# Kernel tuning notes

Hardware: AMD Instinct MI355X
Metric: run time of the kernel (lower is better)

Reference implementation:

```python
import jax, jax.numpy as jnp
import numpy as np

B, L, H, N2, NLAYERS = 8, 4096, 256, 32, 4


def setup_inputs() -> dict:
    key = jax.random.key(0)
    ks = jax.random.split(key, 7)
    x = jax.random.normal(ks[0], (B, L, H), dtype=jnp.float32)
    # S4D kernel params (per layer, stacked on leading dim)
    dt_min, dt_max = 1e-3, 1e-1
    u = jax.random.uniform(ks[1], (NLAYERS, H), dtype=jnp.float32)
    log_dt = u * (np.log(dt_max) - np.log(dt_min)) + np.log(dt_min)
    log_A_real = jnp.log(0.5 * jnp.ones((NLAYERS, H, N2), jnp.float32))
    A_imag = jnp.broadcast_to(np.pi * jnp.arange(N2, dtype=jnp.float32), (NLAYERS, H, N2)) * jnp.ones((NLAYERS, H, N2), jnp.float32)
    C_re = jax.random.normal(ks[2], (NLAYERS, H, N2), dtype=jnp.float32) * (0.5 ** 0.5)
    C_im = jax.random.normal(ks[3], (NLAYERS, H, N2), dtype=jnp.float32) * (0.5 ** 0.5)
    D = jax.random.normal(ks[4], (NLAYERS, H), dtype=jnp.float32)
    Wout = jax.random.normal(ks[5], (NLAYERS, 2 * H, H), dtype=jnp.float32) * (1.0 / H) ** 0.5
    bout = jnp.zeros((NLAYERS, 2 * H), jnp.float32)
    ln_g = jnp.ones((NLAYERS, H), jnp.float32)
    ln_b = jnp.zeros((NLAYERS, H), jnp.float32)
    return dict(x=x, log_dt=log_dt, log_A_real=log_A_real, A_imag=A_imag,
                C_re=C_re, C_im=C_im, D=D, Wout=Wout, bout=bout,
                ln_g=ln_g, ln_b=ln_b)


def _s4d_kernel(log_dt, log_A_real, A_imag, C_re, C_im, Lseq):
    # Vandermonde kernel of S4D: k[h,l] = 2*Re sum_n C'_hn exp(dt_h*A_hn*l)
    dt = jnp.exp(log_dt)                       # (H,)
    A = (-jnp.exp(log_A_real) + 1j * A_imag)   # (H,N) complex
    C = C_re + 1j * C_im                       # (H,N)
    dtA = A * dt[:, None]                      # (H,N)
    K = jnp.exp(dtA[:, :, None] * jnp.arange(Lseq, dtype=jnp.float32))  # (H,N,L)
    Cm = C * (jnp.exp(dtA) - 1.0) / A          # ZOH discretization of C
    return 2.0 * jnp.einsum('hn,hnl->hl', Cm, K).real  # (H,L)


def _s4d_layer(u, log_dt, log_A_real, A_imag, C_re, C_im, D, Wout, bout):
    # u: (B,H,L)
    Lq = u.shape[-1]
    k = _s4d_kernel(log_dt, log_A_real, A_imag, C_re, C_im, Lq)  # (H,L)
    kf = jnp.fft.rfft(k, n=2 * Lq)             # (H, L+1)
    uf = jnp.fft.rfft(u, n=2 * Lq)             # (B,H,L+1)
    y = jnp.fft.irfft(uf * kf, n=2 * Lq)[..., :Lq]
    y = y + u * D[:, None]
    y = jax.nn.gelu(y, approximate=False)
    # output linear: 1x1 conv H->2H followed by GLU along channel dim
    y = jnp.einsum('oh,bhl->bol', Wout, y) + bout[None, :, None]
    a, b = jnp.split(y, 2, axis=1)
    return a * jax.nn.sigmoid(b)               # (B,H,L)


def _layernorm_ch(x, g, b, eps=1e-5):
    # x: (B,H,L); normalize over channel axis H (matches norm on (B,L,H))
    m = jnp.mean(x, axis=1, keepdims=True)
    v = jnp.mean((x - m) ** 2, axis=1, keepdims=True)
    return (x - m) / jnp.sqrt(v + eps) * g[None, :, None] + b[None, :, None]


def reference(x, log_dt, log_A_real, A_imag, C_re, C_im, D, Wout, bout, ln_g, ln_b):
    u = jnp.swapaxes(x, -1, -2)  # (B,H,L)
    for i in range(NLAYERS):  # post-norm (prenorm=False), dropout=identity (eval)
        z = _s4d_layer(u, log_dt[i], log_A_real[i], A_imag[i], C_re[i], C_im[i],
                       D[i], Wout[i], bout[i])
        u = z + u
        u = _layernorm_ch(u, ln_g[i], ln_b[i])
    return jnp.swapaxes(u, -1, -2)  # (B,L,H)
```

## Files before the change

### kernel.cpp

```cpp
#include <hip/hip_runtime.h>
#include <math.h>

#define B    8
#define L    4096
#define H    256
#define N2   32
#define NL   4
#define O2   512
#define BLK  64
#define NBLK 64
#define TVP  136
#define MJP  72
#define UTP  72
#define INP  68
#define TL2  64
#define YPAD 264
#define URP  72

typedef __attribute__((ext_vector_type(8))) short short8;
typedef __attribute__((ext_vector_type(4))) float f32x4;

__device__ __forceinline__ unsigned short f2bf(float f)
{
    unsigned int u = __float_as_uint(f);
    unsigned int r = (u + 0x7fffu + ((u >> 16) & 1u)) >> 16;
    return (unsigned short)r;
}

__device__ __forceinline__ float bf2f(unsigned short v)
{
    return __uint_as_float(((unsigned int)v) << 16);
}

__device__ __forceinline__ float gelu_f(float x)
{
    float t = 1.59576912161f * fmaf(0.044715f * x * x, x, x);
    return x / (1.f + __expf(-t));
}

__global__ __launch_bounds__(256) void k_setup(
    const float* __restrict__ x, const float* __restrict__ log_dt,
    const float* __restrict__ log_Ar, const float* __restrict__ A_im,
    const float* __restrict__ C_re, const float* __restrict__ C_im,
    const float* __restrict__ Dv, const float* __restrict__ Wout,
    unsigned short* __restrict__ Wb, unsigned short* __restrict__ TVc,
    unsigned short* __restrict__ Mm, float2* __restrict__ w64c,
    unsigned short* __restrict__ u)
{
    __shared__ __align__(16) unsigned char smem_raw[27648];
    const int bid = blockIdx.x;
    const int t = threadIdx.x;

    if (bid < 512) {
        int idx = (bid * 256 + t) * 4;
        float4 v = *(const float4*)(Wout + idx);
        ushort4 o;
        o.x = f2bf(v.x); o.y = f2bf(v.y); o.z = f2bf(v.z); o.w = f2bf(v.w);
        *(ushort4*)(Wb + idx) = o;
    } else if (bid < 1536) {
        unsigned short* tvS = (unsigned short*)smem_raw;
        unsigned short* mmS = tvS + BLK * TVP;
        float* kbS = (float*)(mmS + BLK * MJP);
        float* cS  = kbS + BLK;
        const int id = bid - 512;
        const int layer = id >> 8, h = id & 255;
        if (t < 32) {
            const int n0 = t;
            const int idx = (layer * H + h) * N2 + n0;
            double dt = exp((double)log_dt[layer * H + h]);
            double Ar = -exp((double)log_Ar[idx]);
            double Ai = (double)A_im[idx];
            double dtr = dt * Ar, dti = dt * Ai;
            double er = exp(dtr);
            double dwr = er * cos(dti), dwi = er * sin(dti);
            double numr = dwr - 1.0, numi = dwi;
            double den = Ar * Ar + Ai * Ai;
            double qr0 = (numr * Ar + numi * Ai) / den;
            double qi0 = (numi * Ar - numr * Ai) / den;
            double dcr = (double)C_re[idx], dci = (double)C_im[idx];
            cS[n0]       = (float)(2.0 * (dcr * qr0 - dci * qi0));
            cS[32 + n0]  = (float)(2.0 * (dcr * qi0 + dci * qr0));
            cS[64 + n0]  = (float)dwr;
            cS[96 + n0]  = (float)dwi;
            double rev = dti * 0.15915494309189535;
            cS[128 + n0] = (float)(rev - floor(rev));
            cS[160 + n0] = (float)dtr;
            double m64 = exp(64.0 * dtr);
            double a64 = 64.0 * dti;
            w64c[(layer * H + h) * N2 + n0] =
                make_float2((float)(m64 * cos(a64)), (float)(m64 * sin(a64)));
        }
        __syncthreads();
        const int n = t & 31, dg = t >> 5;
        const float cr = cS[n], ci = cS[32 + n];
        const float wr = cS[64 + n], wi = cS[96 + n];
        const float revf = cS[128 + n], dtrf = cS[160 + n];
#pragma unroll
        for (int i = 0; i < 8; ++i) {
            const int d = dg * 8 + i;
            float ph = (float)d * revf;
            ph = (ph - floorf(ph)) * 6.28318530718f;
            float mag = __expf((float)d * dtrf);
            float vr = mag * __cosf(ph);
            float vi = mag * __sinf(ph);
            float pk = fmaf(cr, vr, -(ci * vi));
            pk += __shfl_xor(pk, 1);  pk += __shfl_xor(pk, 2);
            pk += __shfl_xor(pk, 4);  pk += __shfl_xor(pk, 8);
            pk += __shfl_xor(pk, 16);
            if (n == 0) kbS[d] = pk;
            mmS[n * MJP + (63 - d)]        = f2bf(vr);
            mmS[(32 + n) * MJP + (63 - d)] = f2bf(vi);
            float v1r = vr * wr - vi * wi;
            float v1i = vr * wi + vi * wr;
            tvS[d * TVP + 64 + n] = f2bf(fmaf(cr, v1r, -(ci * v1i)));
            tvS[d * TVP + 96 + n] = f2bf(-fmaf(cr, v1i, ci * v1r));
        }
        __syncthreads();
        {
            const int r = t >> 2, c0 = (t & 3) * 16;
            const float diag = kbS[0] + Dv[layer * H + h];
            short8 o8[2];
#pragma unroll
            for (int j = 0; j < 16; ++j) {
                int c = c0 + j;
                float val = (c > r) ? 0.f : ((c == r) ? diag : kbS[r - c]);
                o8[j >> 3][j & 7] = (short)f2bf(val);
            }
            *(short8*)&tvS[r * TVP + c0]     = o8[0];
            *(short8*)&tvS[r * TVP + c0 + 8] = o8[1];
        }
        __syncthreads();
        unsigned short* tv = TVc + (size_t)(layer * H + h) * BLK * TVP;
        unsigned short* mm = Mm + (size_t)(layer * H + h) * BLK * MJP;
        for (int c = t; c < (BLK * TVP) / 8; c += 256)
            *(short8*)(tv + c * 8) = *(const short8*)&tvS[c * 8];
        for (int c = t; c < (BLK * MJP) / 8; c += 256)
            *(short8*)(mm + c * 8) = *(const short8*)&mmS[c * 8];
    } else {
        float* sh = (float*)smem_raw;
        const int rb = bid - 1536;
        const int hx = rb & 7, ly = (rb >> 3) & 63, b = rb >> 9;
        const int h0 = hx * 32, l0 = ly * 64;
        const int tx = t & 7, ty = t >> 3;
        const float* xb = x + ((size_t)b * L + l0) * H + h0;
#pragma unroll
        for (int i = 0; i < 2; ++i) {
            int l = ty + i * 32;
            float4 v = *(const float4*)(xb + (size_t)l * H + tx * 4);
            sh[(tx * 4 + 0) * 68 + l] = v.x;
            sh[(tx * 4 + 1) * 68 + l] = v.y;
            sh[(tx * 4 + 2) * 68 + l] = v.z;
            sh[(tx * 4 + 3) * 68 + l] = v.w;
        }
        __syncthreads();
        const int hh = t >> 3, cc = (t & 7) * 8;
        const float* row = &sh[hh * 68 + cc];
        short8 o8;
#pragma unroll
        for (int j = 0; j < 8; ++j) o8[j] = (short)f2bf(row[j]);
        *(short8*)(u + ((size_t)b * H + h0 + hh) * L + l0 + cc) = o8;
    }
}

__global__ __launch_bounds__(256) void k_scan3(
    const unsigned short* __restrict__ u, const unsigned short* __restrict__ Mm_l,
    const unsigned short* __restrict__ TVc_l, const float2* __restrict__ w64c_l,
    unsigned short* __restrict__ y)
{
    __shared__ __align__(16) unsigned short uT[BLK * UTP];
    __shared__ __align__(16) unsigned short ST[BLK * UTP];
    __shared__ __align__(16) float INC[BLK * INP];
    __shared__ float2 cLd[4][32];
    const int t = threadIdx.x;
    const int wv = t >> 6, lane = t & 63;
    const int lanei = lane & 15, quad = lane >> 4;
    const int h = blockIdx.x >> 3, ct = blockIdx.x & 7;
    const unsigned short* ub = u + (size_t)(ct * H + h) * L;

    const unsigned short* arowA = Mm_l + (size_t)h * BLK * MJP + (wv * 16 + lanei) * MJP + quad * 8;
    short8 mA[2];
    mA[0] = *(const short8*)(arowA);
    mA[1] = *(const short8*)(arowA + 32);
    const unsigned short* arowB = TVc_l + (size_t)h * BLK * TVP + (wv * 16 + lanei) * TVP + quad * 8;
    short8 tB[4];
#pragma unroll
    for (int kt = 0; kt < 4; ++kt)
        tB[kt] = *(const short8*)(arowB + kt * 32);
    const float2 w64 = w64c_l[h * N2 + (lane & 31)];

    {
        int col = t >> 2, q = t & 3;
        *(short8*)&uT[col * UTP + q * 16]     = *(const short8*)(ub + col * 64 + q * 16);
        *(short8*)&uT[col * UTP + q * 16 + 8] = *(const short8*)(ub + col * 64 + q * 16 + 8);
    }
    __syncthreads();

    {
        f32x4 acc[4];
#pragma unroll
        for (int nt = 0; nt < 4; ++nt) acc[nt] = (f32x4){0.f, 0.f, 0.f, 0.f};
#pragma unroll
        for (int kt = 0; kt < 2; ++kt) {
#pragma unroll
            for (int nt = 0; nt < 4; ++nt) {
                short8 b8 = *(const short8*)&uT[(nt * 16 + lanei) * UTP + kt * 32 + quad * 8];
                acc[nt] = __builtin_amdgcn_mfma_f32_16x16x32_bf16(mA[kt], b8, acc[nt], 0, 0, 0);
            }
        }
#pragma unroll
        for (int nt = 0; nt < 4; ++nt)
            *(f32x4*)&INC[(nt * 16 + lanei) * INP + wv * 16 + quad * 4] = acc[nt];
    }
    __syncthreads();

    const int n = lane & 31;
    float Pr[16], Pi[16];
    float w1r = 1.f, w1i = 0.f;
    if (lane < 32) {
        float sr = 0.f, si = 0.f;
        const int base = wv * 16;
#pragma unroll
        for (int k = 0; k < 16; ++k) {
            Pr[k] = sr; Pi[k] = si;
            float ir = INC[(base + k) * INP + n];
            float ii = INC[(base + k) * INP + 32 + n];
            float nr = fmaf(w64.x, sr, fmaf(-w64.y, si, ir));
            float ni = fmaf(w64.x, si, fmaf(w64.y, sr, ii));
            sr = nr; si = ni;
        }
        cLd[wv][n] = make_float2(sr, si);
        float ar = w64.x, ai = w64.y;
#pragma unroll
        for (int q = 0; q < 4; ++q) {
            float nr2 = ar * ar - ai * ai;
            float ni2 = 2.f * ar * ai;
            ar = nr2; ai = ni2;
        }
        w1r = ar; w1i = ai;
    }
    __syncthreads();
    if (lane < 32) {
        float Cr = 0.f, Ci = 0.f;
        for (int wp = 0; wp < wv; ++wp) {
            float2 Lw = cLd[wp][n];
            float nr = fmaf(w1r, Cr, fmaf(-w1i, Ci, Lw.x));
            float ni = fmaf(w1r, Ci, fmaf(w1i, Cr, Lw.y));
            Cr = nr; Ci = ni;
        }
        float pr = 1.f, pi = 0.f;
#pragma unroll
        for (int k = 0; k < 16; ++k) {
            int blk = wv * 16 + k;
            float Sr = fmaf(pr, Cr, fmaf(-pi, Ci, Pr[k]));
            float Si = fmaf(pr, Ci, fmaf(pi, Cr, Pi[k]));
            ST[blk * UTP + n]      = f2bf(Sr);
            ST[blk * UTP + 32 + n] = f2bf(Si);
            float npr = pr * w64.x - pi * w64.y;
            float npi = pr * w64.y + pi * w64.x;
            pr = npr; pi = npi;
        }
    }
    __syncthreads();

    {
        f32x4 acc[4];
#pragma unroll
        for (int nt = 0; nt < 4; ++nt) acc[nt] = (f32x4){0.f, 0.f, 0.f, 0.f};
#pragma unroll
        for (int kt = 0; kt < 4; ++kt) {
            const unsigned short* bb = (kt < 2) ? uT : ST;
            int ko = (kt & 1) * 32 + quad * 8;
#pragma unroll
            for (int nt = 0; nt < 4; ++nt) {
                short8 b8 = *(const short8*)&bb[(nt * 16 + lanei) * UTP + ko];
                acc[nt] = __builtin_amdgcn_mfma_f32_16x16x32_bf16(tB[kt], b8, acc[nt], 0, 0, 0);
            }
        }
        unsigned short* yb = y + (size_t)(ct * H + h) * L;
#pragma unroll
        for (int nt = 0; nt < 4; ++nt) {
            int blk = nt * 16 + lanei;
            int i0 = wv * 16 + quad * 4;
            ushort4 o4;
            o4.x = f2bf(gelu_f(acc[nt][0]));
            o4.y = f2bf(gelu_f(acc[nt][1]));
            o4.z = f2bf(gelu_f(acc[nt][2]));
            o4.w = f2bf(gelu_f(acc[nt][3]));
            *(ushort4*)(yb + blk * 64 + i0) = o4;
        }
    }
}

__global__ __launch_bounds__(512, 4) void k_gemm(
    const unsigned short* __restrict__ y, unsigned short* __restrict__ u,
    const unsigned short* __restrict__ Wb, const float* __restrict__ bo,
    const float* __restrict__ lng, const float* __restrict__ lnb,
    float* __restrict__ outp)
{
    __shared__ __align__(16) unsigned short yS[H * URP];
    __shared__ float bS[O2];
    __shared__ float lgS[H], lbS[H];
    __shared__ float redS[8][4][16], redQ[8][4][16];

    const int t = threadIdx.x;
    const int wv = t >> 6;
    const int lane = t & 63;
    const int lanei = lane & 15;
    const int quad = lane >> 4;
    const int b = blockIdx.x >> 6;
    const int l0 = (blockIdx.x & 63) * TL2;

    size_t abase[2][2];
#pragma unroll
    for (int p = 0; p < 2; ++p)
#pragma unroll
        for (int jj = 0; jj < 2; ++jj)
            abase[p][jj] = (size_t)(p * 256 + wv * 32 + jj * 16 + lanei) * H + quad * 8;

    short8 a8p[4];
#pragma unroll
    for (int p = 0; p < 2; ++p)
#pragma unroll
        for (int jj = 0; jj < 2; ++jj)
            a8p[p * 2 + jj] = *(const short8*)(Wb + abase[p][jj]);

    {
        const int i = t & 7, hr = t >> 3;
        const unsigned short* yb = y + (size_t)b * H * L + l0 + i * 8;
#pragma unroll
        for (int ps = 0; ps < 4; ++ps) {
            int h = ps * 64 + hr;
            short8 v8 = *(const short8*)(yb + (size_t)h * L);
#pragma unroll
            for (int r = 0; r < 8; ++r)
                yS[(i * 8 + r) * YPAD + (h ^ (8 * i))] = (unsigned short)v8[r];
        }
        if (t < O2) bS[t] = bo[t];
        if (t < H) { lgS[t] = lng[t]; lbS[t] = lnb[t]; }
    }
    __syncthreads();

    f32x4 acc[2][2][4];
#pragma unroll
    for (int p = 0; p < 2; ++p)
#pragma unroll
        for (int jj = 0; jj < 2; ++jj)
#pragma unroll
            for (int nt = 0; nt < 4; ++nt)
                acc[p][jj][nt] = (f32x4){0.f, 0.f, 0.f, 0.f};

#pragma unroll
    for (int kt = 0; kt < 8; ++kt) {
        short8 bfr[4];
#pragma unroll
        for (int nt = 0; nt < 4; ++nt) {
            int lp = nt * 16 + lanei;
            int a = (2 * nt + (lanei >> 3)) & 7;
            bfr[nt] = *(const short8*)&yS[lp * YPAD + ((kt * 32 + quad * 8) ^ (8 * a))];
        }
#pragma unroll
        for (int p = 0; p < 2; ++p)
#pragma unroll
            for (int jj = 0; jj < 2; ++jj) {
                short8 a8 = (kt == 0) ? a8p[p * 2 + jj]
                                      : *(const short8*)(Wb + abase[p][jj] + kt * 32);
#pragma unroll
                for (int nt = 0; nt < 4; ++nt)
                    acc[p][jj][nt] = __builtin_amdgcn_mfma_f32_16x16x32_bf16(
                        a8, bfr[nt], acc[p][jj][nt], 0, 0, 0);
            }
    }
    __syncthreads();

    unsigned short* ub = u + (size_t)b * H * L + l0;
#pragma unroll
    for (int r = 0; r < 4; ++r) {
        int c = r * 512 + t;
        int o = c >> 3, c8 = (c & 7) * 8;
        *(short8*)&yS[o * URP + c8] = *(const short8*)(ub + (size_t)o * L + c8);
    }
    __syncthreads();

    float psum[4] = {0.f, 0.f, 0.f, 0.f}, psq[4] = {0.f, 0.f, 0.f, 0.f};
#pragma unroll
    for (int jj = 0; jj < 2; ++jj) {
#pragma unroll
        for (int nt = 0; nt < 4; ++nt) {
            int lc = nt * 16 + lanei;
#pragma unroll
            for (int reg = 0; reg < 4; ++reg) {
                int o = wv * 32 + jj * 16 + quad * 4 + reg;
                float a = acc[0][jj][nt][reg] + bS[o];
                float g = acc[1][jj][nt][reg] + bS[o + 256];
                float glu = a / (1.f + __expf(-g));
                float val = glu + bf2f(yS[o * URP + lc]);
                acc[0][jj][nt][reg] = val;
                psum[nt] += val;
                psq[nt] = fmaf(val, val, psq[nt]);
            }
        }
    }
#pragma unroll
    for (int nt = 0; nt < 4; ++nt) {
        psum[nt] += __shfl_xor(psum[nt], 16);
        psum[nt] += __shfl_xor(psum[nt], 32);
        psq[nt]  += __shfl_xor(psq[nt], 16);
        psq[nt]  += __shfl_xor(psq[nt], 32);
    }
    if (lane < 16) {
#pragma unroll
        for (int nt = 0; nt < 4; ++nt) {
            redS[wv][nt][lanei] = psum[nt];
            redQ[wv][nt][lanei] = psq[nt];
        }
    }
    __syncthreads();
    float mcol[4], icol[4];
#pragma unroll
    for (int nt = 0; nt < 4; ++nt) {
        float s = 0.f, q = 0.f;
#pragma unroll
        for (int w = 0; w < 8; ++w) { s += redS[w][nt][lanei]; q += redQ[w][nt][lanei]; }
        float m = s * (1.0f / 256.0f);
        float v = q * (1.0f / 256.0f) - m * m;
        mcol[nt] = m;
        icol[nt] = rsqrtf(v + 1e-5f);
    }
    if (outp == nullptr) {
#pragma unroll
        for (int jj = 0; jj < 2; ++jj) {
#pragma unroll
            for (int nt = 0; nt < 4; ++nt) {
                int lc = nt * 16 + lanei;
#pragma unroll
                for (int reg = 0; reg < 4; ++reg) {
                    int o = wv * 32 + jj * 16 + quad * 4 + reg;
                    float val = acc[0][jj][nt][reg];
                    float ov = (val - mcol[nt]) * icol[nt] * lgS[o] + lbS[o];
                    yS[o * URP + lc] = f2bf(ov);
                }
            }
        }
        __syncthreads();
#pragma unroll
        for (int r = 0; r < 4; ++r) {
            int c = r * 512 + t;
            int o = c >> 3, c8 = (c & 7) * 8;
            *(short8*)(ub + (size_t)o * L + c8) = *(const short8*)&yS[o * URP + c8];
        }
    } else {
#pragma unroll
        for (int jj = 0; jj < 2; ++jj) {
#pragma unroll
            for (int nt = 0; nt < 4; ++nt) {
                int lc = nt * 16 + lanei;
                int o0 = wv * 32 + jj * 16 + quad * 4;
                float4 ov;
#pragma unroll
                for (int reg = 0; reg < 4; ++reg) {
                    int o = o0 + reg;
                    float val = acc[0][jj][nt][reg];
                    ((float*)&ov)[reg] = (val - mcol[nt]) * icol[nt] * lgS[o] + lbS[o];
                }
                *(float4*)(outp + ((size_t)b * L + l0 + lc) * H + o0) = ov;
            }
        }
    }
}

extern "C" void kernel_launch(void* const* d_in, const int* in_sizes, int n_in,
                              void* d_out, int out_size, void* d_ws, size_t ws_size,
                              hipStream_t stream)
{
    const float* x      = (const float*)d_in[0];
    const float* log_dt = (const float*)d_in[1];
    const float* log_Ar = (const float*)d_in[2];
    const float* A_im   = (const float*)d_in[3];
    const float* C_re   = (const float*)d_in[4];
    const float* C_im   = (const float*)d_in[5];
    const float* Dv     = (const float*)d_in[6];
    const float* Wout   = (const float*)d_in[7];
    const float* bout   = (const float*)d_in[8];
    const float* lng    = (const float*)d_in[9];
    const float* lnb    = (const float*)d_in[10];
    float* out = (float*)d_out;

    unsigned short* u   = (unsigned short*)d_ws;
    unsigned short* Wb  = u + (size_t)B * H * L;
    unsigned short* TVc = Wb + (size_t)NL * O2 * H;
    unsigned short* Mm  = TVc + (size_t)NL * H * BLK * TVP;
    float2* w64c        = (float2*)(Mm + (size_t)NL * H * BLK * MJP);
    unsigned short* y   = (unsigned short*)(w64c + (size_t)NL * H * N2);

    k_setup<<<5632, 256, 0, stream>>>(x, log_dt, log_Ar, A_im, C_re, C_im, Dv, Wout,
                                      Wb, TVc, Mm, w64c, u);
    for (int layer = 0; layer < NL; ++layer) {
        k_scan3<<<H * 8, 256, 0, stream>>>(u, Mm + (size_t)layer * H * BLK * MJP,
                                           TVc + (size_t)layer * H * BLK * TVP,
                                           w64c + (size_t)layer * H * N2, y);
        k_gemm<<<B * L / TL2, 512, 0, stream>>>(y, u, Wb + (size_t)layer * O2 * H,
                                                bout + layer * O2, lng + layer * H, lnb + layer * H,
                                                (layer == NL - 1) ? out : nullptr);
    }
}
```

Baseline: 298.9 us.

## Halve GEMM L-tile to 32 with 256-thread blocks; stage scan output via LDS

The GEMM/GLU/LayerNorm kernel now uses 32-column L tiles with 256 threads, each wave covering 64 output channels. That doubles the grid and cuts per-block LDS, which may raise occupancy, but W is reloaded twice as often. The scan kernel now writes its gelu output to shared memory and stores it to global as coalesced 16-byte vectors instead of scattered 8-byte stores. This adds two barriers.

```diff
diff --git a/kernel.cpp b/kernel.cpp
--- a/kernel.cpp
+++ b/kernel.cpp
@@ -13,9 +13,9 @@
 #define MJP  72
 #define UTP  72
 #define INP  68
-#define TL2  64
+#define TL2  32
 #define YPAD 264
-#define URP  72
+#define URP2 40
 
 typedef __attribute__((ext_vector_type(8))) short short8;
 typedef __attribute__((ext_vector_type(4))) float f32x4;
@@ -276,7 +276,7 @@
                 acc[nt] = __builtin_amdgcn_mfma_f32_16x16x32_bf16(tB[kt], b8, acc[nt], 0, 0, 0);
             }
         }
-        unsigned short* yb = y + (size_t)(ct * H + h) * L;
+        __syncthreads();
 #pragma unroll
         for (int nt = 0; nt < 4; ++nt) {
             int blk = nt * 16 + lanei;
@@ -286,46 +286,47 @@
             o4.y = f2bf(gelu_f(acc[nt][1]));
             o4.z = f2bf(gelu_f(acc[nt][2]));
             o4.w = f2bf(gelu_f(acc[nt][3]));
-            *(ushort4*)(yb + blk * 64 + i0) = o4;
-        }
-    }
-}
-
-__global__ __launch_bounds__(512, 4) void k_gemm(
+            *(ushort4*)&uT[blk * UTP + i0] = o4;
+        }
+        __syncthreads();
+        unsigned short* yb = y + (size_t)(ct * H + h) * L;
+#pragma unroll
+        for (int r = 0; r < 2; ++r) {
+            int c = r * 256 + t;
+            int o = c >> 3, c8 = (c & 7) * 8;
+            *(short8*)(yb + o * 64 + c8) = *(const short8*)&uT[o * UTP + c8];
+        }
+    }
+}
+
+__global__ __launch_bounds__(256, 4) void k_gemm(
     const unsigned short* __restrict__ y, unsigned short* __restrict__ u,
     const unsigned short* __restrict__ Wb, const float* __restrict__ bo,
     const float* __restrict__ lng, const float* __restrict__ lnb,
     float* __restrict__ outp)
 {
-    __shared__ __align__(16) unsigned short yS[H * URP];
+    __shared__ __align__(16) unsigned short yS[10240];
     __shared__ float bS[O2];
     __shared__ float lgS[H], lbS[H];
-    __shared__ float redS[8][4][16], redQ[8][4][16];
+    __shared__ float redS[4][2][16], redQ[4][2][16];
 
     const int t = threadIdx.x;
     const int wv = t >> 6;
     const int lane = t & 63;
     const int lanei = lane & 15;
     const int quad = lane >> 4;
-    const int b = blockIdx.x >> 6;
-    const int l0 = (blockIdx.x & 63) * TL2;
-
-    size_t abase[2][2];
+    const int b = blockIdx.x >> 7;
+    const int l0 = (blockIdx.x & 127) * TL2;
+
+    size_t abase[2][4];
 #pragma unroll
     for (int p = 0; p < 2; ++p)
 #pragma unroll
-        for (int jj = 0; jj < 2; ++jj)
-            abase[p][jj] = (size_t)(p * 256 + wv * 32 + jj * 16 + lanei) * H + quad * 8;
-
-    short8 a8p[4];
-#pragma unroll
-    for (int p = 0; p < 2; ++p)
-#pragma unroll
-        for (int jj = 0; jj < 2; ++jj)
-            a8p[p * 2 + jj] = *(const short8*)(Wb + abase[p][jj]);
+        for (int jj = 0; jj < 4; ++jj)
+            abase[p][jj] = (size_t)(p * 256 + wv * 64 + jj * 16 + lanei) * H + quad * 8;
 
     {
-        const int i = t & 7, hr = t >> 3;
+        const int i = t & 3, hr = t >> 2;
         const unsigned short* yb = y + (size_t)b * H * L + l0 + i * 8;
 #pragma unroll
         for (int ps = 0; ps < 4; ++ps) {
@@ -335,25 +336,26 @@
             for (int r = 0; r < 8; ++r)
                 yS[(i * 8 + r) * YPAD + (h ^ (8 * i))] = (unsigned short)v8[r];
         }
-        if (t < O2) bS[t] = bo[t];
-        if (t < H) { lgS[t] = lng[t]; lbS[t] = lnb[t]; }
-    }
-    __syncthreads();
-
-    f32x4 acc[2][2][4];
+        bS[t] = bo[t];
+        bS[t + 256] = bo[t + 256];
+        lgS[t] = lng[t]; lbS[t] = lnb[t];
+    }
+    __syncthreads();
+
+    f32x4 acc[2][4][2];
 #pragma unroll
     for (int p = 0; p < 2; ++p)
 #pragma unroll
-        for (int jj = 0; jj < 2; ++jj)
-#pragma unroll
-            for (int nt = 0; nt < 4; ++nt)
+        for (int jj = 0; jj < 4; ++jj)
+#pragma unroll
+            for (int nt = 0; nt < 2; ++nt)
                 acc[p][jj][nt] = (f32x4){0.f, 0.f, 0.f, 0.f};
 
 #pragma unroll
     for (int kt = 0; kt < 8; ++kt) {
-        short8 bfr[4];
-#pragma unroll
-        for (int nt = 0; nt < 4; ++nt) {
+        short8 bfr[2];
+#pragma unroll
+        for (int nt = 0; nt < 2; ++nt) {
             int lp = nt * 16 + lanei;
             int a = (2 * nt + (lanei >> 3)) & 7;
             bfr[nt] = *(const short8*)&yS[lp * YPAD + ((kt * 32 + quad * 8) ^ (8 * a))];
@@ -361,11 +363,10 @@
 #pragma unroll
         for (int p = 0; p < 2; ++p)
 #pragma unroll
-            for (int jj = 0; jj < 2; ++jj) {
-                short8 a8 = (kt == 0) ? a8p[p * 2 + jj]
-                                      : *(const short8*)(Wb + abase[p][jj] + kt * 32);
-#pragma unroll
-                for (int nt = 0; nt < 4; ++nt)
+            for (int jj = 0; jj < 4; ++jj) {
+                short8 a8 = *(const short8*)(Wb + abase[p][jj] + kt * 32);
+#pragma unroll
+                for (int nt = 0; nt < 2; ++nt)
                     acc[p][jj][nt] = __builtin_amdgcn_mfma_f32_16x16x32_bf16(
                         a8, bfr[nt], acc[p][jj][nt], 0, 0, 0);
             }
@@ -375,25 +376,25 @@
     unsigned short* ub = u + (size_t)b * H * L + l0;
 #pragma unroll
     for (int r = 0; r < 4; ++r) {
-        int c = r * 512 + t;
-        int o = c >> 3, c8 = (c & 7) * 8;
-        *(short8*)&yS[o * URP + c8] = *(const short8*)(ub + (size_t)o * L + c8);
-    }
-    __syncthreads();
-
-    float psum[4] = {0.f, 0.f, 0.f, 0.f}, psq[4] = {0.f, 0.f, 0.f, 0.f};
-#pragma unroll
-    for (int jj = 0; jj < 2; ++jj) {
-#pragma unroll
-        for (int nt = 0; nt < 4; ++nt) {
+        int c = r * 256 + t;
+        int o = c >> 2, c8 = (c & 3) * 8;
+        *(short8*)&yS[o * URP2 + c8] = *(const short8*)(ub + (size_t)o * L + c8);
+    }
+    __syncthreads();
+
+    float psum[2] = {0.f, 0.f}, psq[2] = {0.f, 0.f};
+#pragma unroll
+    for (int jj = 0; jj < 4; ++jj) {
+#pragma unroll
+        for (int nt = 0; nt < 2; ++nt) {
             int lc = nt * 16 + lanei;
 #pragma unroll
             for (int reg = 0; reg < 4; ++reg) {
-                int o = wv * 32 + jj * 16 + quad * 4 + reg;
+                int o = wv * 64 + jj * 16 + quad * 4 + reg;
                 float a = acc[0][jj][nt][reg] + bS[o];
                 float g = acc[1][jj][nt][reg] + bS[o + 256];
                 float glu = a / (1.f + __expf(-g));
-                float val = glu + bf2f(yS[o * URP + lc]);
+                float val = glu + bf2f(yS[o * URP2 + lc]);
                 acc[0][jj][nt][reg] = val;
                 psum[nt] += val;
                 psq[nt] = fmaf(val, val, psq[nt]);
@@ -401,7 +402,7 @@
         }
     }
 #pragma unroll
-    for (int nt = 0; nt < 4; ++nt) {
+    for (int nt = 0; nt < 2; ++nt) {
         psum[nt] += __shfl_xor(psum[nt], 16);
         psum[nt] += __shfl_xor(psum[nt], 32);
         psq[nt]  += __shfl_xor(psq[nt], 16);
@@ -409,18 +410,18 @@
     }
     if (lane < 16) {
 #pragma unroll
-        for (int nt = 0; nt < 4; ++nt) {
+        for (int nt = 0; nt < 2; ++nt) {
             redS[wv][nt][lanei] = psum[nt];
             redQ[wv][nt][lanei] = psq[nt];
         }
     }
     __syncthreads();
-    float mcol[4], icol[4];
-#pragma unroll
-    for (int nt = 0; nt < 4; ++nt) {
+    float mcol[2], icol[2];
+#pragma unroll
+    for (int nt = 0; nt < 2; ++nt) {
         float s = 0.f, q = 0.f;
 #pragma unroll
-        for (int w = 0; w < 8; ++w) { s += redS[w][nt][lanei]; q += redQ[w][nt][lanei]; }
+        for (int w = 0; w < 4; ++w) { s += redS[w][nt][lanei]; q += redQ[w][nt][lanei]; }
         float m = s * (1.0f / 256.0f);
         float v = q * (1.0f / 256.0f) - m * m;
         mcol[nt] = m;
@@ -428,33 +429,33 @@
     }
     if (outp == nullptr) {
 #pragma unroll
-        for (int jj = 0; jj < 2; ++jj) {
-#pragma unroll
-            for (int nt = 0; nt < 4; ++nt) {
+        for (int jj = 0; jj < 4; ++jj) {
+#pragma unroll
+            for (int nt = 0; nt < 2; ++nt) {
                 int lc = nt * 16 + lanei;
 #pragma unroll
                 for (int reg = 0; reg < 4; ++reg) {
-                    int o = wv * 32 + jj * 16 + quad * 4 + reg;
+                    int o = wv * 64 + jj * 16 + quad * 4 + reg;
                     float val = acc[0][jj][nt][reg];
                     float ov = (val - mcol[nt]) * icol[nt] * lgS[o] + lbS[o];
-                    yS[o * URP + lc] = f2bf(ov);
+                    yS[o * URP2 + lc] = f2bf(ov);
                 }
             }
         }
         __syncthreads();
 #pragma unroll
         for (int r = 0; r < 4; ++r) {
-            int c = r * 512 + t;
-            int o = c >> 3, c8 = (c & 7) * 8;
-            *(short8*)(ub + (size_t)o * L + c8) = *(const short8*)&yS[o * URP + c8];
+            int c = r * 256 + t;
+            int o = c >> 2, c8 = (c & 3) * 8;
+            *(short8*)(ub + (size_t)o * L + c8) = *(const short8*)&yS[o * URP2 + c8];
         }
     } else {
 #pragma unroll
-        for (int jj = 0; jj < 2; ++jj) {
-#pragma unroll
-            for (int nt = 0; nt < 4; ++nt) {
+        for (int jj = 0; jj < 4; ++jj) {
+#pragma unroll
+            for (int nt = 0; nt < 2; ++nt) {
                 int lc = nt * 16 + lanei;
-                int o0 = wv * 32 + jj * 16 + quad * 4;
+                int o0 = wv * 64 + jj * 16 + quad * 4;
                 float4 ov;
 #pragma unroll
                 for (int reg = 0; reg < 4; ++reg) {
@@ -498,7 +499,7 @@
         k_scan3<<<H * 8, 256, 0, stream>>>(u, Mm + (size_t)layer * H * BLK * MJP,
                                            TVc + (size_t)layer * H * BLK * TVP,
                                            w64c + (size_t)layer * H * N2, y);
-        k_gemm<<<B * L / TL2, 512, 0, stream>>>(y, u, Wb + (size_t)layer * O2 * H,
+        k_gemm<<<B * L / TL2, 256, 0, stream>>>(y, u, Wb + (size_t)layer * O2 * H,
                                                 bout + layer * O2, lng + layer * H, lnb + layer * H,
                                                 (layer == NL - 1) ? out : nullptr);
     }
```

Result: slower. 360.7 us (+20.7%).
